# Kernel optimization log

Measured on AMD Instinct MI355X. Metric: run time of the kernel, lower is better.

## Reference

```python
import jax, jax.numpy as jnp
import numpy as np

COS_EPS = 1e-8  # torch.nn.CosineSimilarity default eps
B, L, D = 32, 512, 1024
S, E = 256, 64
POS = 17


def _padded_idxs(key, batch, max_len, seq_len, min_frac=0.5):
    """Random first-subword indices in [1, seq_len) with trailing zero padding."""
    k1, k2 = jax.random.split(key)
    lens = jax.random.randint(k1, (batch,), int(max_len * min_frac), max_len + 1)
    vals = jax.random.randint(k2, (batch, max_len), 1, seq_len)
    col = jnp.arange(max_len)[None, :]
    return jnp.where(col < lens[:, None], vals, 0).astype(jnp.int32)


def setup_inputs() -> dict:
    key = jax.random.key(0)
    ks = jax.random.split(key, 7)
    all_embeddings = jax.random.normal(ks[0], (B, L, D), dtype=jnp.float32)
    W = jax.random.uniform(ks[1], (D, D), dtype=jnp.float32) / np.sqrt(D)
    lin_w = jax.random.normal(ks[2], (2, 2 * D + POS), dtype=jnp.float32) * 0.02
    lin_b = jnp.zeros((2,), dtype=jnp.float32)
    idxs_to_collect_sent = _padded_idxs(ks[3], B, S, L)
    idxs_to_collect_event = _padded_idxs(ks[4], B, E, L)
    pos_tag = jax.random.randint(ks[5], (B, S), -1, POS - 1).astype(jnp.int32)
    return {
        "all_embeddings": all_embeddings,
        "W": W,
        "lin_w": lin_w,
        "lin_b": lin_b,
        "idxs_to_collect_sent": idxs_to_collect_sent,
        "idxs_to_collect_event": idxs_to_collect_event,
        "pos_tag": pos_tag,
    }


def _gather_pad(all_embeddings, idxs):
    # idxs has valid (>0) entries at the front, zeros as trailing pad, so the
    # per-sample compact-gather-then-pad loop is equivalent to gather + mask.
    mask = (idxs > 0)  # [B, T]
    gathered = jnp.take_along_axis(
        all_embeddings, jnp.maximum(idxs, 0)[..., None], axis=1)  # [B, T, D]
    return gathered * mask[..., None].astype(all_embeddings.dtype), mask


def reference(all_embeddings, W, lin_w, lin_b,
              idxs_to_collect_sent, idxs_to_collect_event, pos_tag):
    sent, _ = _gather_pad(all_embeddings, idxs_to_collect_sent)       # [B,S,D]
    event, ev_mask = _gather_pad(all_embeddings, idxs_to_collect_event)  # [B,E,D]

    # map_numerator = 1 / number of valid event tokens per sample
    map_num = 1.0 / jnp.sum(ev_mask, axis=-1).astype(sent.dtype)  # [B]

    # cosine similarity between (sent @ W) and event embeddings
    a = jnp.einsum('bsd,de->bse', sent, W)                 # [B,S,D]
    num = jnp.einsum('bsd,bed->bse', a, event)             # [B,S,E]
    na = jnp.maximum(jnp.linalg.norm(a, axis=-1), COS_EPS)       # [B,S]
    ne = jnp.maximum(jnp.linalg.norm(event, axis=-1), COS_EPS)   # [B,E]
    logits = num / (na[:, :, None] * ne[:, None, :])       # [B,S,E]

    sent2event_att = jnp.einsum('bse,bed->bsd', logits, event) * map_num[:, None, None]

    pos = jnp.where(pos_tag < 0, POS - 1, pos_tag)
    pos_oh = jax.nn.one_hot(pos, POS, dtype=sent.dtype)    # [B,S,17]

    feat = jnp.concatenate([sent, sent2event_att, pos_oh], axis=-1)  # [B,S,2D+17]
    return feat @ lin_w.T + lin_b                           # [B,S,2]
```

## Files before the change

kernel.cpp:

```cpp
#include <hip/hip_runtime.h>

#define B_ 32
#define L_ 512
#define D_ 1024
#define S_ 256
#define E_ 64
#define POS_ 17
#define LWS 2065
#define M_ (B_*S_)

typedef __attribute__((ext_vector_type(8))) short short8v;
typedef __attribute__((ext_vector_type(4))) float f32x4;
typedef __attribute__((ext_vector_type(16))) float f32x16;
typedef __attribute__((ext_vector_type(4))) unsigned short us4;

__device__ __forceinline__ unsigned short f2bf(float x) {
  union { float f; unsigned u; } v; v.f = x;
  unsigned r = v.u + 0x7FFFu + ((v.u >> 16) & 1u);
  return (unsigned short)(r >> 16);
}
__device__ __forceinline__ float bf2f(unsigned short b) {
  union { unsigned u; float f; } v; v.u = ((unsigned)b) << 16;
  return v.f;
}
__device__ __forceinline__ void async16(void* lds, const void* g) {
  __builtin_amdgcn_global_load_lds(
      (const __attribute__((address_space(1))) unsigned int*)(unsigned long long)g,
      (__attribute__((address_space(3))) unsigned int*)(unsigned int)(unsigned long long)lds,
      16, 0, 0);
}

#define VMCNT6 asm volatile("s_waitcnt vmcnt(6)" ::: "memory")
#define VMCNT0 asm volatile("s_waitcnt vmcnt(0)" ::: "memory")
#define BARRIER __builtin_amdgcn_s_barrier()

__global__ __launch_bounds__(256) void prep_all(
    const float* __restrict__ emb, const float* __restrict__ W,
    const float* __restrict__ lin_w, const float* __restrict__ lin_b,
    const int* __restrict__ idx_s, const int* __restrict__ idx_e,
    const int* __restrict__ pos_tag,
    unsigned short* __restrict__ sentb, unsigned short* __restrict__ evb,
    unsigned short* __restrict__ Wt,
    float* __restrict__ base, float* __restrict__ ne, float* __restrict__ evw) {
  int bid = blockIdx.x;
  int t = threadIdx.x;

  if (bid >= 2560) {
    __shared__ float tile[32][33];
    int tt = bid - 2560;
    int bx = tt & 31, by = tt >> 5;
    int tx = t & 31, ty = t >> 5;
#pragma unroll
    for (int i = 0; i < 4; i++)
      tile[ty + i * 8][tx] = W[(size_t)(by * 32 + ty + i * 8) * D_ + bx * 32 + tx];
    __syncthreads();
#pragma unroll
    for (int i = 0; i < 4; i++)
      Wt[(size_t)(bx * 32 + ty + i * 8) * D_ + by * 32 + tx] = f2bf(tile[tx][ty + i * 8]);
    return;
  }

  int lane = t & 63, w = t >> 6;
  bool is_sent = bid < 2048;
  int row = is_sent ? (((bid & 7) << 10) | ((bid >> 3) << 2) | w)
                    : (((bid - 2048) << 2) | w);
  int b = is_sent ? (row >> 8) : (row >> 6);
  int idx = is_sent ? idx_s[row] : idx_e[row];
  float msk = idx > 0 ? 1.0f : 0.0f;
  const float* src = emb + ((size_t)b * L_ + (idx > 0 ? idx : 0)) * D_;

  float r0 = 0.f, r1 = 0.f, sq = 0.f;
  const float* lw0 = is_sent ? lin_w : (lin_w + D_);
  const float* lw1 = is_sent ? (lin_w + LWS) : (lin_w + LWS + D_);
  unsigned short* dst = is_sent ? (sentb + (size_t)row * D_)
                                : (evb + (size_t)row * D_);
#pragma unroll
  for (int j = 0; j < 4; j++) {
    int d = j * 256 + lane * 4;
    float4 v = *(const float4*)(src + d);
    v.x *= msk; v.y *= msk; v.z *= msk; v.w *= msk;
    us4 o; o.x = f2bf(v.x); o.y = f2bf(v.y); o.z = f2bf(v.z); o.w = f2bf(v.w);
    *(us4*)&dst[d] = o;
    float4 c0 = *(const float4*)(lw0 + d);
    float4 c1 = *(const float4*)(lw1 + d);
    r0 += v.x * c0.x + v.y * c0.y + v.z * c0.z + v.w * c0.w;
    r1 += v.x * c1.x + v.y * c1.y + v.z * c1.z + v.w * c1.w;
    if (!is_sent) sq += v.x * v.x + v.y * v.y + v.z * v.z + v.w * v.w;
  }
#pragma unroll
  for (int off = 32; off; off >>= 1) {
    r0 += __shfl_xor(r0, off);
    r1 += __shfl_xor(r1, off);
  }
  if (is_sent) {
    if (lane == 0) {
      int p = pos_tag[row]; if (p < 0) p = POS_ - 1;
      base[(size_t)row * 2 + 0] = r0 + lin_b[0] + lin_w[2 * D_ + p];
      base[(size_t)row * 2 + 1] = r1 + lin_b[1] + lin_w[LWS + 2 * D_ + p];
    }
  } else {
#pragma unroll
    for (int off = 32; off; off >>= 1) sq += __shfl_xor(sq, off);
    if (lane == 0) {
      ne[row] = fmaxf(sqrtf(sq), 1e-8f);
      evw[(size_t)row * 2 + 0] = r0;
      evw[(size_t)row * 2 + 1] = r1;
    }
  }
}

__device__ __forceinline__ void stage_g(const char* gA, const char* gB,
    unsigned short* bA, unsigned short* bB, int t, int kt) {
  int sc = ((t & 7) ^ ((t >> 3) & 7)) << 4;
#pragma unroll
  for (int i = 0; i < 4; i++) {
    int row = i * 64 + (t >> 3);
    size_t src = (size_t)row * (D_ * 2) + (size_t)kt * 128 + sc;
    async16((char*)bA + i * 8192 + t * 16, gA + src);
  }
#pragma unroll
  for (int i = 0; i < 2; i++) {
    int row = i * 64 + (t >> 3);
    size_t src = (size_t)row * (D_ * 2) + (size_t)kt * 128 + sc;
    async16((char*)bB + i * 8192 + t * 16, gB + src);
  }
}
__device__ __forceinline__ void comp_g(const unsigned short* bA,
    const unsigned short* bB, f32x16 (&acc)[2][2], int wr, int wc, int fr32, int hi1) {
  int x = fr32 & 7;
#pragma unroll
  for (int ks = 0; ks < 4; ks++) {
    int co = ((ks * 2 + hi1) ^ x) << 3;
    short8v a[2], bv[2];
#pragma unroll
    for (int m = 0; m < 2; m++)
      a[m] = *(const short8v*)&bA[(wr * 64 + m * 32 + fr32) * 64 + co];
#pragma unroll
    for (int n = 0; n < 2; n++)
      bv[n] = *(const short8v*)&bB[(wc * 64 + n * 32 + fr32) * 64 + co];
#pragma unroll
    for (int m = 0; m < 2; m++)
#pragma unroll
      for (int n = 0; n < 2; n++)
        acc[m][n] = __builtin_amdgcn_mfma_f32_32x32x16_bf16(a[m], bv[n], acc[m][n], 0, 0, 0);
  }
}

__global__ __launch_bounds__(512) void gemm_aw(
    const unsigned short* __restrict__ A,
    const unsigned short* __restrict__ Bt,
    unsigned short* __restrict__ C) {
  const int K = D_, N = D_;
  __shared__ unsigned short sA0[256 * 64], sA1[256 * 64];
  __shared__ unsigned short sB0[128 * 64], sB1[128 * 64];
  int t = threadIdx.x;
  int w = t >> 6, lane = t & 63;
  int wr = w >> 1, wc = w & 1;
  int fr32 = lane & 31, hi1 = lane >> 5;
  int bid = blockIdx.x;
  int wg = ((bid & 7) << 5) | (bid >> 3);
  int n0 = (wg & 7) * 128, m0 = (wg >> 3) * 256;
  f32x16 acc[2][2];
#pragma unroll
  for (int m = 0; m < 2; m++)
#pragma unroll
    for (int n = 0; n < 2; n++)
#pragma unroll
      for (int r = 0; r < 16; r++) acc[m][n][r] = 0.f;

  const char* gA = (const char*)(A + (size_t)m0 * K);
  const char* gB = (const char*)(Bt + (size_t)n0 * K);

  stage_g(gA, gB, sA0, sB0, t, 0);
#pragma unroll 1
  for (int kt = 0; kt < 14; kt += 2) {
    stage_g(gA, gB, sA1, sB1, t, kt + 1);
    VMCNT6; BARRIER;
    __builtin_amdgcn_sched_barrier(0);
    comp_g(sA0, sB0, acc, wr, wc, fr32, hi1);
    BARRIER;
    stage_g(gA, gB, sA0, sB0, t, kt + 2);
    VMCNT6; BARRIER;
    __builtin_amdgcn_sched_barrier(0);
    comp_g(sA1, sB1, acc, wr, wc, fr32, hi1);
    BARRIER;
  }
  stage_g(gA, gB, sA1, sB1, t, 15);
  VMCNT6; BARRIER;
  __builtin_amdgcn_sched_barrier(0);
  comp_g(sA0, sB0, acc, wr, wc, fr32, hi1);
  VMCNT0; BARRIER;
  __builtin_amdgcn_sched_barrier(0);
  comp_g(sA1, sB1, acc, wr, wc, fr32, hi1);

#pragma unroll
  for (int m = 0; m < 2; m++) {
#pragma unroll
    for (int n = 0; n < 2; n++) {
#pragma unroll
      for (int r = 0; r < 16; r++) {
        int crow = (r & 3) + 8 * (r >> 2) + 4 * hi1;
        int row = wr * 64 + m * 32 + crow;
        C[(size_t)(m0 + row) * N + n0 + wc * 64 + n * 32 + fr32] = f2bf(acc[m][n][r]);
      }
    }
  }
}

__device__ __forceinline__ void stage_a(const char* gA, const char* gE,
    unsigned short* bA, unsigned short* bE, int t, int kt) {
#pragma unroll
  for (int i = 0; i < 2; i++) {
    int idx = i * 256 + t;
    int row = idx >> 4;
    int ch = (idx & 15) ^ (row & 15);
    async16((char*)bA + idx * 16, gA + (size_t)row * (D_ * 2) + (size_t)kt * 256 + ch * 16);
  }
#pragma unroll
  for (int i = 0; i < 4; i++) {
    int idx = i * 256 + t;
    int row = idx >> 4;
    int ch = (idx & 15) ^ (row & 15);
    async16((char*)bE + idx * 16, gE + (size_t)row * (D_ * 2) + (size_t)kt * 256 + ch * 16);
  }
}
__device__ __forceinline__ void comp_a(const unsigned short* bA,
    const unsigned short* bE, f32x4 (&acc)[2], float& rsq, int w, int fr, int hi) {
  int rowA = (w >> 1) * 16 + fr;
  int ch = w & 1;
#pragma unroll
  for (int ks = 0; ks < 4; ks++) {
    int ca = ((ks * 4 + hi) ^ (rowA & 15)) << 3;
    short8v af = *(const short8v*)&bA[rowA * 128 + ca];
    if (ch == 0) {
#pragma unroll
      for (int j = 0; j < 8; j++) { float xv = bf2f((unsigned short)af[j]); rsq += xv * xv; }
    }
#pragma unroll
    for (int n = 0; n < 2; n++) {
      int rowE = ch * 32 + n * 16 + fr;
      int ce = ((ks * 4 + hi) ^ (rowE & 15)) << 3;
      short8v bv = *(const short8v*)&bE[rowE * 128 + ce];
      acc[n] = __builtin_amdgcn_mfma_f32_16x16x32_bf16(af, bv, acc[n], 0, 0, 0);
    }
  }
}

__global__ __launch_bounds__(256) void attn_ep(
    const unsigned short* __restrict__ Abf,
    const unsigned short* __restrict__ Ebf,
    const int* __restrict__ idx_e,
    const float* __restrict__ ne, const float* __restrict__ evw,
    const float* __restrict__ base,
    float* __restrict__ out) {
  int bid = blockIdx.x;
  int xcd = bid & 7, loc = bid >> 3;
  int b = xcd * 4 + (loc >> 3);
  int s0 = (loc & 7) * 32;
  __shared__ unsigned short sA0[32 * 128], sA1[32 * 128];
  __shared__ unsigned short sE0[64 * 128], sE1[64 * 128];
  __shared__ float sRne[E_], sEvw[E_][2], sRna[32], sP[2][32][2];
  __shared__ float sMapn;
  int t = threadIdx.x;
  int w = t >> 6, lane = t & 63;
  int fr = lane & 15, hi = lane >> 4;
  if (t < E_) {
    sRne[t] = 1.0f / ne[b * E_ + t];
    sEvw[t][0] = evw[(size_t)(b * E_ + t) * 2 + 0];
    sEvw[t][1] = evw[(size_t)(b * E_ + t) * 2 + 1];
    unsigned long long mball = __ballot(idx_e[b * E_ + t] > 0);
    if (t == 0) sMapn = 1.0f / (float)__popcll(mball);
  }
  f32x4 acc[2];
#pragma unroll
  for (int n = 0; n < 2; n++) acc[n] = f32x4{0.f, 0.f, 0.f, 0.f};
  float rsq = 0.f;

  const char* gA = (const char*)(Abf + ((size_t)b * S_ + s0) * D_);
  const char* gE = (const char*)(Ebf + (size_t)b * E_ * D_);

  stage_a(gA, gE, sA0, sE0, t, 0);
  __syncthreads();
#pragma unroll 1
  for (int kt = 0; kt < 8; kt += 2) {
    stage_a(gA, gE, sA1, sE1, t, kt + 1);
    comp_a(sA0, sE0, acc, rsq, w, fr, hi);
    __syncthreads();
    if (kt + 2 < 8) stage_a(gA, gE, sA0, sE0, t, kt + 2);
    comp_a(sA1, sE1, acc, rsq, w, fr, hi);
    __syncthreads();
  }
  rsq += __shfl_xor(rsq, 16);
  rsq += __shfl_xor(rsq, 32);
  if ((w & 1) == 0 && lane < 16)
    sRna[(w >> 1) * 16 + lane] = 1.0f / fmaxf(sqrtf(rsq), 1e-8f);
  __syncthreads();

  int ch = w & 1;
#pragma unroll
  for (int r = 0; r < 4; r++) {
    int srl = (w >> 1) * 16 + hi * 4 + r;
    float rna = sRna[srl];
    float a0 = 0.f, a1 = 0.f;
#pragma unroll
    for (int n = 0; n < 2; n++) {
      int e = ch * 32 + n * 16 + fr;
      float lg = acc[n][r] * rna * sRne[e];
      a0 += lg * sEvw[e][0];
      a1 += lg * sEvw[e][1];
    }
#pragma unroll
    for (int off = 1; off < 16; off <<= 1) {
      a0 += __shfl_xor(a0, off);
      a1 += __shfl_xor(a1, off);
    }
    if (fr == 0) { sP[ch][srl][0] = a0; sP[ch][srl][1] = a1; }
  }
  __syncthreads();
  if (t < 64) {
    int row = t >> 1, c = t & 1;
    float v = sP[0][row][c] + sP[1][row][c];
    size_t sg = (size_t)b * S_ + s0 + row;
    out[sg * 2 + c] = base[sg * 2 + c] + sMapn * v;
  }
}

extern "C" void kernel_launch(void* const* d_in, const int* in_sizes, int n_in,
                              void* d_out, int out_size, void* d_ws, size_t ws_size,
                              hipStream_t stream) {
  const float* emb   = (const float*)d_in[0];
  const float* W     = (const float*)d_in[1];
  const float* lin_w = (const float*)d_in[2];
  const float* lin_b = (const float*)d_in[3];
  const int* idx_s   = (const int*)d_in[4];
  const int* idx_e   = (const int*)d_in[5];
  const int* pos     = (const int*)d_in[6];
  float* out = (float*)d_out;

  char* ws = (char*)d_ws;
  const size_t MB = 1024 * 1024;
  unsigned short* sentb = (unsigned short*)(ws);
  unsigned short* abf   = (unsigned short*)(ws + 16 * MB);
  unsigned short* evb   = (unsigned short*)(ws + 32 * MB);
  unsigned short* Wt    = (unsigned short*)(ws + 36 * MB);
  float* ne   = (float*)(ws + 38 * MB);
  float* evw  = ne + 2048;
  float* base = evw + 4096;

  prep_all<<<3584, 256, 0, stream>>>(
      emb, W, lin_w, lin_b, idx_s, idx_e, pos, sentb, evb, Wt, base, ne, evw);
  gemm_aw<<<256, 512, 0, stream>>>(sentb, Wt, abf);
  attn_ep<<<B_ * 8, 256, 0, stream>>>(abf, evb, idx_e, ne, evw, base, out);
}
```

Measured before the change: 43.38 us.

## Triple-buffer LDS in gemm_aw to drop one barrier per k-step

```diff
diff --git a/kernel.cpp b/kernel.cpp
--- a/kernel.cpp
+++ b/kernel.cpp
@@ -30,8 +30,6 @@
       16, 0, 0);
 }
 
-#define VMCNT6 asm volatile("s_waitcnt vmcnt(6)" ::: "memory")
-#define VMCNT0 asm volatile("s_waitcnt vmcnt(0)" ::: "memory")
 #define BARRIER __builtin_amdgcn_s_barrier()
 
 __global__ __launch_bounds__(256) void prep_all(
@@ -146,13 +144,20 @@
   }
 }
 
+#define GBODY(CNT, bA, bB, nA, nB, KT, ISSUE)                        \
+  asm volatile("s_waitcnt vmcnt(" #CNT ")" ::: "memory");            \
+  BARRIER;                                                           \
+  __builtin_amdgcn_sched_barrier(0);                                 \
+  if (ISSUE) stage_g(gA, gB, nA, nB, t, (KT) + 2);                   \
+  comp_g(bA, bB, acc, wr, wc, fr32, hi1);
+
 __global__ __launch_bounds__(512) void gemm_aw(
     const unsigned short* __restrict__ A,
     const unsigned short* __restrict__ Bt,
     unsigned short* __restrict__ C) {
   const int K = D_, N = D_;
-  __shared__ unsigned short sA0[256 * 64], sA1[256 * 64];
-  __shared__ unsigned short sB0[128 * 64], sB1[128 * 64];
+  __shared__ unsigned short sA0[256 * 64], sA1[256 * 64], sA2[256 * 64];
+  __shared__ unsigned short sB0[128 * 64], sB1[128 * 64], sB2[128 * 64];
   int t = threadIdx.x;
   int w = t >> 6, lane = t & 63;
   int wr = w >> 1, wc = w & 1;
@@ -172,26 +177,17 @@
   const char* gB = (const char*)(Bt + (size_t)n0 * K);
 
   stage_g(gA, gB, sA0, sB0, t, 0);
+  stage_g(gA, gB, sA1, sB1, t, 1);
 #pragma unroll 1
-  for (int kt = 0; kt < 14; kt += 2) {
-    stage_g(gA, gB, sA1, sB1, t, kt + 1);
-    VMCNT6; BARRIER;
-    __builtin_amdgcn_sched_barrier(0);
-    comp_g(sA0, sB0, acc, wr, wc, fr32, hi1);
-    BARRIER;
-    stage_g(gA, gB, sA0, sB0, t, kt + 2);
-    VMCNT6; BARRIER;
-    __builtin_amdgcn_sched_barrier(0);
-    comp_g(sA1, sB1, acc, wr, wc, fr32, hi1);
-    BARRIER;
-  }
-  stage_g(gA, gB, sA1, sB1, t, 15);
-  VMCNT6; BARRIER;
-  __builtin_amdgcn_sched_barrier(0);
-  comp_g(sA0, sB0, acc, wr, wc, fr32, hi1);
-  VMCNT0; BARRIER;
-  __builtin_amdgcn_sched_barrier(0);
-  comp_g(sA1, sB1, acc, wr, wc, fr32, hi1);
+  for (int g = 0; g < 12; g += 3) {
+    GBODY(6, sA0, sB0, sA2, sB2, g,     true);
+    GBODY(6, sA1, sB1, sA0, sB0, g + 1, true);
+    GBODY(6, sA2, sB2, sA1, sB1, g + 2, true);
+  }
+  GBODY(6, sA0, sB0, sA2, sB2, 12, true);
+  GBODY(6, sA1, sB1, sA0, sB0, 13, true);
+  GBODY(6, sA2, sB2, sA1, sB1, 14, false);
+  GBODY(0, sA0, sB0, sA2, sB2, 15, false);
 
 #pragma unroll
   for (int m = 0; m < 2; m++) {
```

After: 44.01 us. No clear change (+1.4%).

## Fuse A·Eᵀ partial products and row norms into the A=sent·W GEMM epilogue

Applied to the files above, without the earlier changes.

```diff
diff --git a/kernel.cpp b/kernel.cpp
--- a/kernel.cpp
+++ b/kernel.cpp
@@ -146,20 +146,31 @@
   }
 }
 
-__global__ __launch_bounds__(512) void gemm_aw(
+__global__ __launch_bounds__(512) void gemm_fused(
     const unsigned short* __restrict__ A,
     const unsigned short* __restrict__ Bt,
-    unsigned short* __restrict__ C) {
-  const int K = D_, N = D_;
-  __shared__ unsigned short sA0[256 * 64], sA1[256 * 64];
-  __shared__ unsigned short sB0[128 * 64], sB1[128 * 64];
+    const unsigned short* __restrict__ evb,
+    unsigned short* __restrict__ pnum,
+    float* __restrict__ prsq) {
+  const int K = D_;
+  __shared__ __align__(16) char pool[98304];
+  unsigned short* sA0 = (unsigned short*)pool;
+  unsigned short* sA1 = (unsigned short*)(pool + 32768);
+  unsigned short* sB0 = (unsigned short*)(pool + 65536);
+  unsigned short* sB1 = (unsigned short*)(pool + 81920);
+  char* aT  = pool;
+  char* sEv = pool + 65536;
+  float (*sRq)[256] = (float(*)[256])(pool + 81920);
+
   int t = threadIdx.x;
   int w = t >> 6, lane = t & 63;
   int wr = w >> 1, wc = w & 1;
   int fr32 = lane & 31, hi1 = lane >> 5;
   int bid = blockIdx.x;
   int wg = ((bid & 7) << 5) | (bid >> 3);
-  int n0 = (wg & 7) * 128, m0 = (wg >> 3) * 256;
+  int ns = wg & 7;
+  int bb = wg >> 3;
+  int n0 = ns * 128, m0 = bb * 256;
   f32x16 acc[2][2];
 #pragma unroll
   for (int m = 0; m < 2; m++)
@@ -193,135 +204,109 @@
   __builtin_amdgcn_sched_barrier(0);
   comp_g(sA1, sB1, acc, wr, wc, fr32, hi1);
 
-#pragma unroll
-  for (int m = 0; m < 2; m++) {
+  __syncthreads();
+
+#pragma unroll
+  for (int m = 0; m < 2; m++)
+#pragma unroll
+    for (int n = 0; n < 2; n++)
+#pragma unroll
+      for (int r = 0; r < 16; r++) {
+        int row = wr * 64 + m * 32 + (r & 3) + 8 * (r >> 2) + 4 * hi1;
+        int col = wc * 64 + n * 32 + fr32;
+        int ch = (col >> 3) ^ (row & 15);
+        *(unsigned short*)(aT + row * 256 + ch * 16 + (col & 7) * 2) =
+            f2bf(acc[m][n][r]);
+      }
+#pragma unroll
+  for (int m = 0; m < 2; m++)
+#pragma unroll
+    for (int r = 0; r < 16; r++) {
+      float s = acc[m][0][r] * acc[m][0][r] + acc[m][1][r] * acc[m][1][r];
+#pragma unroll
+      for (int off = 1; off <= 16; off <<= 1) s += __shfl_xor(s, off);
+      if (fr32 == 0)
+        sRq[wc][wr * 64 + m * 32 + (r & 3) + 8 * (r >> 2) + 4 * hi1] = s;
+    }
+  {
+    const char* gEv = (const char*)(evb + (size_t)bb * E_ * D_ + n0);
+#pragma unroll
+    for (int i = 0; i < 2; i++) {
+      int idx = i * 512 + t;
+      int row = idx >> 4;
+      int ch = (idx & 15) ^ (row & 15);
+      async16(sEv + idx * 16, gEv + (size_t)row * (D_ * 2) + ch * 16);
+    }
+  }
+  VMCNT0;
+  __syncthreads();
+
+  f32x16 acc2[2];
+#pragma unroll
+  for (int n = 0; n < 2; n++)
+#pragma unroll
+    for (int r = 0; r < 16; r++) acc2[n][r] = 0.f;
+  int row2 = w * 32 + fr32;
+#pragma unroll
+  for (int ks = 0; ks < 8; ks++) {
+    short8v av = *(const short8v*)(aT + row2 * 256 +
+                                   ((ks * 2 + hi1) ^ (row2 & 15)) * 16);
 #pragma unroll
     for (int n = 0; n < 2; n++) {
+      int e = n * 32 + fr32;
+      short8v bv = *(const short8v*)(sEv + e * 256 +
+                                     ((ks * 2 + hi1) ^ (e & 15)) * 16);
+      acc2[n] = __builtin_amdgcn_mfma_f32_32x32x16_bf16(av, bv, acc2[n], 0, 0, 0);
+    }
+  }
+  {
+    unsigned short* pn = pnum + ((size_t)ns * M_ + bb * 256 + w * 32) * 64;
+#pragma unroll
+    for (int n = 0; n < 2; n++)
 #pragma unroll
       for (int r = 0; r < 16; r++) {
-        int crow = (r & 3) + 8 * (r >> 2) + 4 * hi1;
-        int row = wr * 64 + m * 32 + crow;
-        C[(size_t)(m0 + row) * N + n0 + wc * 64 + n * 32 + fr32] = f2bf(acc[m][n][r]);
+        int rr = (r & 3) + 8 * (r >> 2) + 4 * hi1;
+        pn[(size_t)rr * 64 + n * 32 + fr32] = f2bf(acc2[n][r]);
       }
-    }
-  }
-}
-
-__device__ __forceinline__ void stage_a(const char* gA, const char* gE,
-    unsigned short* bA, unsigned short* bE, int t, int kt) {
-#pragma unroll
-  for (int i = 0; i < 2; i++) {
-    int idx = i * 256 + t;
-    int row = idx >> 4;
-    int ch = (idx & 15) ^ (row & 15);
-    async16((char*)bA + idx * 16, gA + (size_t)row * (D_ * 2) + (size_t)kt * 256 + ch * 16);
-  }
-#pragma unroll
-  for (int i = 0; i < 4; i++) {
-    int idx = i * 256 + t;
-    int row = idx >> 4;
-    int ch = (idx & 15) ^ (row & 15);
-    async16((char*)bE + idx * 16, gE + (size_t)row * (D_ * 2) + (size_t)kt * 256 + ch * 16);
-  }
-}
-__device__ __forceinline__ void comp_a(const unsigned short* bA,
-    const unsigned short* bE, f32x4 (&acc)[2], float& rsq, int w, int fr, int hi) {
-  int rowA = (w >> 1) * 16 + fr;
-  int ch = w & 1;
-#pragma unroll
-  for (int ks = 0; ks < 4; ks++) {
-    int ca = ((ks * 4 + hi) ^ (rowA & 15)) << 3;
-    short8v af = *(const short8v*)&bA[rowA * 128 + ca];
-    if (ch == 0) {
-#pragma unroll
-      for (int j = 0; j < 8; j++) { float xv = bf2f((unsigned short)af[j]); rsq += xv * xv; }
-    }
-#pragma unroll
-    for (int n = 0; n < 2; n++) {
-      int rowE = ch * 32 + n * 16 + fr;
-      int ce = ((ks * 4 + hi) ^ (rowE & 15)) << 3;
-      short8v bv = *(const short8v*)&bE[rowE * 128 + ce];
-      acc[n] = __builtin_amdgcn_mfma_f32_16x16x32_bf16(af, bv, acc[n], 0, 0, 0);
-    }
-  }
-}
-
-__global__ __launch_bounds__(256) void attn_ep(
-    const unsigned short* __restrict__ Abf,
-    const unsigned short* __restrict__ Ebf,
+  }
+  if (t < 256)
+    prsq[(size_t)ns * M_ + bb * 256 + t] = sRq[0][t] + sRq[1][t];
+}
+
+__global__ __launch_bounds__(256) void attn_fin(
+    const unsigned short* __restrict__ pnum,
+    const float* __restrict__ prsq,
     const int* __restrict__ idx_e,
     const float* __restrict__ ne, const float* __restrict__ evw,
-    const float* __restrict__ base,
-    float* __restrict__ out) {
-  int bid = blockIdx.x;
-  int xcd = bid & 7, loc = bid >> 3;
-  int b = xcd * 4 + (loc >> 3);
-  int s0 = (loc & 7) * 32;
-  __shared__ unsigned short sA0[32 * 128], sA1[32 * 128];
-  __shared__ unsigned short sE0[64 * 128], sE1[64 * 128];
-  __shared__ float sRne[E_], sEvw[E_][2], sRna[32], sP[2][32][2];
-  __shared__ float sMapn;
+    const float* __restrict__ base, float* __restrict__ out) {
   int t = threadIdx.x;
-  int w = t >> 6, lane = t & 63;
-  int fr = lane & 15, hi = lane >> 4;
-  if (t < E_) {
-    sRne[t] = 1.0f / ne[b * E_ + t];
-    sEvw[t][0] = evw[(size_t)(b * E_ + t) * 2 + 0];
-    sEvw[t][1] = evw[(size_t)(b * E_ + t) * 2 + 1];
-    unsigned long long mball = __ballot(idx_e[b * E_ + t] > 0);
-    if (t == 0) sMapn = 1.0f / (float)__popcll(mball);
-  }
-  f32x4 acc[2];
-#pragma unroll
-  for (int n = 0; n < 2; n++) acc[n] = f32x4{0.f, 0.f, 0.f, 0.f};
-  float rsq = 0.f;
-
-  const char* gA = (const char*)(Abf + ((size_t)b * S_ + s0) * D_);
-  const char* gE = (const char*)(Ebf + (size_t)b * E_ * D_);
-
-  stage_a(gA, gE, sA0, sE0, t, 0);
-  __syncthreads();
-#pragma unroll 1
-  for (int kt = 0; kt < 8; kt += 2) {
-    stage_a(gA, gE, sA1, sE1, t, kt + 1);
-    comp_a(sA0, sE0, acc, rsq, w, fr, hi);
-    __syncthreads();
-    if (kt + 2 < 8) stage_a(gA, gE, sA0, sE0, t, kt + 2);
-    comp_a(sA1, sE1, acc, rsq, w, fr, hi);
-    __syncthreads();
-  }
-  rsq += __shfl_xor(rsq, 16);
-  rsq += __shfl_xor(rsq, 32);
-  if ((w & 1) == 0 && lane < 16)
-    sRna[(w >> 1) * 16 + lane] = 1.0f / fmaxf(sqrtf(rsq), 1e-8f);
-  __syncthreads();
-
-  int ch = w & 1;
-#pragma unroll
-  for (int r = 0; r < 4; r++) {
-    int srl = (w >> 1) * 16 + hi * 4 + r;
-    float rna = sRna[srl];
-    float a0 = 0.f, a1 = 0.f;
-#pragma unroll
-    for (int n = 0; n < 2; n++) {
-      int e = ch * 32 + n * 16 + fr;
-      float lg = acc[n][r] * rna * sRne[e];
-      a0 += lg * sEvw[e][0];
-      a1 += lg * sEvw[e][1];
-    }
-#pragma unroll
-    for (int off = 1; off < 16; off <<= 1) {
-      a0 += __shfl_xor(a0, off);
-      a1 += __shfl_xor(a1, off);
-    }
-    if (fr == 0) { sP[ch][srl][0] = a0; sP[ch][srl][1] = a1; }
-  }
-  __syncthreads();
-  if (t < 64) {
-    int row = t >> 1, c = t & 1;
-    float v = sP[0][row][c] + sP[1][row][c];
-    size_t sg = (size_t)b * S_ + s0 + row;
-    out[sg * 2 + c] = base[sg * 2 + c] + sMapn * v;
+  int w = t >> 6, e = t & 63;
+  int row = blockIdx.x * 4 + w;
+  int b = row >> 8;
+  unsigned long long mb = __ballot(idx_e[b * E_ + e] > 0);
+  float mapn = 1.0f / (float)__popcll(mb);
+  float num = 0.f;
+#pragma unroll
+  for (int ns = 0; ns < 8; ns++)
+    num += bf2f(pnum[((size_t)ns * M_ + row) * 64 + e]);
+  float rsq = (e < 8) ? prsq[(size_t)e * M_ + row] : 0.f;
+#pragma unroll
+  for (int off = 1; off < 8; off <<= 1) rsq += __shfl_xor(rsq, off);
+  rsq = __shfl(rsq, 0);
+  float rna = 1.0f / fmaxf(sqrtf(rsq), 1e-8f);
+  float lg = num * rna * (1.0f / ne[b * E_ + e]);
+  float a0 = lg * evw[(size_t)(b * E_ + e) * 2 + 0];
+  float a1 = lg * evw[(size_t)(b * E_ + e) * 2 + 1];
+#pragma unroll
+  for (int off = 1; off < 64; off <<= 1) {
+    a0 += __shfl_xor(a0, off);
+    a1 += __shfl_xor(a1, off);
+  }
+  if (e == 0) {
+    float2 res;
+    res.x = base[(size_t)row * 2 + 0] + mapn * a0;
+    res.y = base[(size_t)row * 2 + 1] + mapn * a1;
+    *(float2*)&out[(size_t)row * 2] = res;
   }
 }
 
@@ -340,7 +325,8 @@
   char* ws = (char*)d_ws;
   const size_t MB = 1024 * 1024;
   unsigned short* sentb = (unsigned short*)(ws);
-  unsigned short* abf   = (unsigned short*)(ws + 16 * MB);
+  unsigned short* pnum  = (unsigned short*)(ws + 16 * MB);
+  float*          prsq  = (float*)(ws + 24 * MB);
   unsigned short* evb   = (unsigned short*)(ws + 32 * MB);
   unsigned short* Wt    = (unsigned short*)(ws + 36 * MB);
   float* ne   = (float*)(ws + 38 * MB);
@@ -349,6 +335,6 @@
 
   prep_all<<<3584, 256, 0, stream>>>(
       emb, W, lin_w, lin_b, idx_s, idx_e, pos, sentb, evb, Wt, base, ne, evw);
-  gemm_aw<<<256, 512, 0, stream>>>(sentb, Wt, abf);
-  attn_ep<<<B_ * 8, 256, 0, stream>>>(abf, evb, idx_e, ne, evw, base, out);
-}
+  gemm_fused<<<256, 512, 0, stream>>>(sentb, Wt, evb, pnum, prsq);
+  attn_fin<<<M_ / 4, 256, 0, stream>>>(pnum, prsq, idx_e, ne, evw, base, out);
+}
```

Measured after the change: 45.11 us. 4.0% more time.
